# Kernel optimization log

Measured on AMD Instinct MI355X. Metric: run time of the kernel, lower is better.

## Reference

```python
import jax, jax.numpy as jnp
import numpy as np

NUM_HEADS = 32
HEAD_DIM = 128
ROPE_THETA = 10000.0


def setup_inputs() -> dict:
    key = jax.random.key(0)
    k1, k2, k3 = jax.random.split(key, 3)
    B, S, H = 2, 2048, 4096
    scale = 0.02
    return {
        "x": jax.random.normal(k1, (B, S, H), dtype=jnp.float32),
        "Wqkv": jax.random.normal(k2, (H, 3 * H), dtype=jnp.float32) * scale,
        "Wo": jax.random.normal(k3, (H, H), dtype=jnp.float32) * scale,
    }


def _rope_cos_sin(seq_len, head_dim, dtype):
    # inv_freq over even dims, llama convention
    inv_freq = 1.0 / (ROPE_THETA ** (jnp.arange(0, head_dim, 2, dtype=jnp.float32) / head_dim))
    t = jnp.arange(seq_len, dtype=jnp.float32)
    freqs = jnp.outer(t, inv_freq)            # [S, hd/2]
    emb = jnp.concatenate([freqs, freqs], -1)  # [S, hd]
    return jnp.cos(emb).astype(dtype), jnp.sin(emb).astype(dtype)


def _rotate_half(v):
    v1, v2 = jnp.split(v, 2, axis=-1)
    return jnp.concatenate([-v2, v1], axis=-1)


def _apply_rope(q, k, cos, sin):
    # q,k: [B,S,nh,hd]; cos,sin: [S,hd] -> broadcast over B and heads
    cos = cos[None, :, None, :]
    sin = sin[None, :, None, :]
    q = q * cos + _rotate_half(q) * sin
    k = k * cos + _rotate_half(k) * sin
    return q, k


def reference(x, Wqkv, Wo):
    B, S, H = x.shape
    nh, hd = NUM_HEADS, HEAD_DIM
    scaling = 1.0 / jnp.sqrt(jnp.asarray(hd, dtype=x.dtype))

    qkv = jnp.einsum("bsh,hk->bsk", x, Wqkv)           # fused QKV proj
    q, k, v = jnp.split(qkv, 3, axis=-1)
    q = q.reshape(B, S, nh, hd)
    k = k.reshape(B, S, nh, hd)
    v = v.reshape(B, S, nh, hd)

    cos, sin = _rope_cos_sin(S, hd, x.dtype)
    q, k = _apply_rope(q, k, cos, sin)

    # causal scaled dot-product attention
    scores = jnp.einsum("bqnd,bknd->bnqk", q, k) * scaling  # [B,nh,S,S]
    causal = jnp.tril(jnp.ones((S, S), dtype=bool))
    scores = jnp.where(causal[None, None], scores, jnp.finfo(scores.dtype).min)
    probs = jax.nn.softmax(scores, axis=-1)
    ctx = jnp.einsum("bnqk,bknd->bqnd", probs, v).reshape(B, S, nh * hd)

    return jnp.einsum("bsh,ho->bso", ctx, Wo)
```

## Files before the change

kernel.cpp:

```cpp
#include <hip/hip_runtime.h>

typedef __bf16 v8bf __attribute__((ext_vector_type(8)));
typedef float  v4f  __attribute__((ext_vector_type(4)));

__device__ __forceinline__ float bf2f(unsigned short h) {
    union { unsigned int u; float f; } x; x.u = ((unsigned int)h) << 16; return x.f;
}
__device__ __forceinline__ unsigned short f2bf(float f) {
    union { float f; unsigned int u; } x; x.f = f;
    unsigned int u = x.u;
    u += 0x7fffu + ((u >> 16) & 1u);
    return (unsigned short)(u >> 16);
}
__device__ __forceinline__ void gll16(const void* g, void* l) {
    __builtin_amdgcn_global_load_lds((__attribute__((address_space(1))) void*)g,
                                     (__attribute__((address_space(3))) void*)l,
                                     16, 0, 0);
}

__global__ __launch_bounds__(256) void cvt_f32_bf16(
    const float* __restrict__ in, unsigned short* __restrict__ out)
{
    size_t i = ((size_t)blockIdx.x * 256 + threadIdx.x) * 4;
    float4 v = *(const float4*)&in[i];
    ushort4 o;
    o.x = f2bf(v.x); o.y = f2bf(v.y); o.z = f2bf(v.z); o.w = f2bf(v.w);
    *(ushort4*)&out[i] = o;
}

__global__ __launch_bounds__(256) void transpose_f32_bf16(
    const float* __restrict__ in, unsigned short* __restrict__ out, int ldIn, int M)
{
    __shared__ unsigned short t[64][68];
    const int c0 = blockIdx.x * 64, r0 = blockIdx.y * 64;
    const int lr = threadIdx.x >> 4;
    const int lc = (threadIdx.x & 15) * 4;
#pragma unroll
    for (int i = 0; i < 4; ++i) {
        int row = lr + i * 16;
        float4 v = *(const float4*)&in[(size_t)(r0 + row) * ldIn + c0 + lc];
        ushort4 o;
        o.x = f2bf(v.x); o.y = f2bf(v.y); o.z = f2bf(v.z); o.w = f2bf(v.w);
        *(ushort4*)&t[row][lc] = o;
    }
    __syncthreads();
#pragma unroll
    for (int i = 0; i < 4; ++i) {
        int orow = lr + i * 16;
        ushort4 v;
        v.x = t[lc + 0][orow]; v.y = t[lc + 1][orow];
        v.z = t[lc + 2][orow]; v.w = t[lc + 3][orow];
        *(ushort4*)&out[(size_t)(c0 + orow) * M + r0 + lc] = v;
    }
}

template <int MODE>
__global__ __launch_bounds__(512, 2) void gemm256(
    const unsigned short* __restrict__ A, const unsigned short* __restrict__ Bt,
    float* __restrict__ Cf, unsigned short* __restrict__ Ov, float postScale)
{
    constexpr int NT = 64;
    __shared__ unsigned short lA[4 * 8192];
    __shared__ unsigned short lB[4 * 8192];
    const int tid = threadIdx.x;
    const int wave = tid >> 6, lane = tid & 63;
    const int quad = lane >> 4, l16 = lane & 15;
    const int wr = wave >> 2, wc = wave & 3;

    const int bid = blockIdx.x;
    const int swz = (bid & 7) * 32 + (bid >> 3);
    const int m0 = (swz >> 4) * 256, n0 = (swz & 15) * 256;

    v4f acc[8][4] = {};

    const int srow = tid >> 3;
    const int sof  = ((tid & 7) ^ (srow & 7)) << 3;
    const unsigned short* pA[2][2]; const unsigned short* pB[2][2];
#pragma unroll
    for (int H = 0; H < 2; ++H)
#pragma unroll
        for (int i = 0; i < 2; ++i) {
            pA[H][i] = A  + (size_t)(m0 + H * 128 + i * 64 + srow) * 4096 + sof;
            pB[H][i] = Bt + (size_t)(n0 + H * 128 + i * 64 + srow) * 4096 + sof;
        }
    const int dst0 = tid * 8;

    auto stA = [&](int H, int kt) {
        unsigned short* d = &lA[((kt & 1) * 2 + H) * 8192 + dst0];
        gll16(pA[H][0] + kt * 64, d);
        gll16(pA[H][1] + kt * 64, d + 4096);
    };
    auto stB = [&](int H, int kt) {
        unsigned short* d = &lB[((kt & 1) * 2 + H) * 8192 + dst0];
        gll16(pB[H][0] + kt * 64, d);
        gll16(pB[H][1] + kt * 64, d + 4096);
    };

    stB(0, 0); stB(1, 0); stA(0, 0); stA(1, 0);
    stB(0, 1); stB(1, 1); stA(0, 1);
    asm volatile("s_waitcnt vmcnt(6)" ::: "memory");
    __builtin_amdgcn_s_barrier();

    const int cko0 = (quad ^ (l16 & 7)) << 3;
    const int cko1 = ((4 + quad) ^ (l16 & 7)) << 3;
    const int arow0 = l16 * 64;
    const int brow0 = (wc * 16 + l16) * 64;

#pragma unroll 2
    for (int t = 0; t < NT; ++t) {
        const int c = t & 1;
        const unsigned short* lAc = &lA[(c * 2 + wr) * 8192];
        const unsigned short* lB0 = &lB[(c * 2 + 0) * 8192];
        const unsigned short* lB1 = &lB[(c * 2 + 1) * 8192];
        v8bf a[4][2], b0[2][2], b1[2][2];

#pragma unroll
        for (int mi = 0; mi < 4; ++mi) {
            a[mi][0] = *(const v8bf*)&lAc[arow0 + mi * 1024 + cko0];
            a[mi][1] = *(const v8bf*)&lAc[arow0 + mi * 1024 + cko1];
        }
#pragma unroll
        for (int ni = 0; ni < 2; ++ni) {
            b0[ni][0] = *(const v8bf*)&lB0[brow0 + ni * 4096 + cko0];
            b0[ni][1] = *(const v8bf*)&lB0[brow0 + ni * 4096 + cko1];
        }
        if (t + 1 < NT) stA(1, t + 1);
        __builtin_amdgcn_s_barrier();
        __builtin_amdgcn_s_setprio(1);
#pragma unroll
        for (int kc = 0; kc < 2; ++kc)
#pragma unroll
            for (int mi = 0; mi < 4; ++mi)
#pragma unroll
                for (int ni = 0; ni < 2; ++ni)
                    acc[mi][ni] = __builtin_amdgcn_mfma_f32_16x16x32_bf16(
                        a[mi][kc], b0[ni][kc], acc[mi][ni], 0, 0, 0);
        __builtin_amdgcn_s_setprio(0);
        __builtin_amdgcn_s_barrier();

#pragma unroll
        for (int ni = 0; ni < 2; ++ni) {
            b1[ni][0] = *(const v8bf*)&lB1[brow0 + ni * 4096 + cko0];
            b1[ni][1] = *(const v8bf*)&lB1[brow0 + ni * 4096 + cko1];
        }
        if (t + 2 < NT) stB(0, t + 2);
        __builtin_amdgcn_s_barrier();
        __builtin_amdgcn_s_setprio(1);
#pragma unroll
        for (int kc = 0; kc < 2; ++kc)
#pragma unroll
            for (int mi = 0; mi < 4; ++mi)
#pragma unroll
                for (int ni = 0; ni < 2; ++ni)
                    acc[mi][2 + ni] = __builtin_amdgcn_mfma_f32_16x16x32_bf16(
                        a[mi][kc], b1[ni][kc], acc[mi][2 + ni], 0, 0, 0);
        __builtin_amdgcn_s_setprio(0);
        __builtin_amdgcn_s_barrier();

#pragma unroll
        for (int mi = 0; mi < 4; ++mi) {
            a[mi][0] = *(const v8bf*)&lAc[arow0 + (4 + mi) * 1024 + cko0];
            a[mi][1] = *(const v8bf*)&lAc[arow0 + (4 + mi) * 1024 + cko1];
        }
        if (t + 2 < NT) stB(1, t + 2);
        __builtin_amdgcn_s_barrier();
        __builtin_amdgcn_s_setprio(1);
#pragma unroll
        for (int kc = 0; kc < 2; ++kc)
#pragma unroll
            for (int mi = 0; mi < 4; ++mi)
#pragma unroll
                for (int ni = 0; ni < 2; ++ni)
                    acc[4 + mi][2 + ni] = __builtin_amdgcn_mfma_f32_16x16x32_bf16(
                        a[mi][kc], b1[ni][kc], acc[4 + mi][2 + ni], 0, 0, 0);
        __builtin_amdgcn_s_setprio(0);
        __builtin_amdgcn_s_barrier();

        if (t + 2 < NT) {
            stA(0, t + 2);
            asm volatile("s_waitcnt vmcnt(6)" ::: "memory");
        } else if (t + 1 < NT) {
            asm volatile("s_waitcnt vmcnt(0)" ::: "memory");
        }
        __builtin_amdgcn_s_barrier();
        __builtin_amdgcn_s_setprio(1);
#pragma unroll
        for (int kc = 0; kc < 2; ++kc)
#pragma unroll
            for (int mi = 0; mi < 4; ++mi)
#pragma unroll
                for (int ni = 0; ni < 2; ++ni)
                    acc[4 + mi][ni] = __builtin_amdgcn_mfma_f32_16x16x32_bf16(
                        a[mi][kc], b0[ni][kc], acc[4 + mi][ni], 0, 0, 0);
        __builtin_amdgcn_s_setprio(0);
        __builtin_amdgcn_s_barrier();
    }

    if (MODE == 0) {
#pragma unroll
        for (int mi = 0; mi < 8; ++mi) {
            int gm = m0 + wr * 128 + mi * 16 + quad * 4;
#pragma unroll
            for (int ni = 0; ni < 4; ++ni) {
                int gn = n0 + ni * 64 + wc * 16 + l16;
#pragma unroll
                for (int r = 0; r < 4; ++r)
                    Cf[(size_t)(gm + r) * 4096 + gn] = acc[mi][ni][r];
            }
        }
    } else if (MODE == 1) {
        const int d1 = wc * 16 + l16;
        const float inv = powf(10000.0f, -(float)d1 * 0.015625f);
        const int head0 = n0 >> 7;
#pragma unroll
        for (int mi = 0; mi < 8; ++mi) {
            int gmb = m0 + wr * 128 + mi * 16 + quad * 4;
            int b = gmb >> 11, sb = gmb & 2047;
            float sn[4], cs[4];
#pragma unroll
            for (int r = 0; r < 4; ++r)
                sincosf((float)(sb + r) * inv, &sn[r], &cs[r]);
#pragma unroll
            for (int hd = 0; hd < 2; ++hd) {
                size_t hb = ((size_t)(b * 32 + head0 + hd)) << 11;
#pragma unroll
                for (int r = 0; r < 4; ++r) {
                    float x1 = acc[mi][2 * hd][r], x2 = acc[mi][2 * hd + 1][r];
                    size_t adr = (hb + sb + r) << 7;
                    Ov[adr + d1]      = f2bf((x1 * cs[r] - x2 * sn[r]) * postScale);
                    Ov[adr + d1 + 64] = f2bf((x2 * cs[r] + x1 * sn[r]) * postScale);
                }
            }
        }
    } else {
        const int head0 = n0 >> 7;
#pragma unroll
        for (int mi = 0; mi < 8; ++mi) {
            int gmb = m0 + wr * 128 + mi * 16 + quad * 4;
            int b = gmb >> 11, s0 = gmb & 2047;
#pragma unroll
            for (int ni = 0; ni < 4; ++ni) {
                int head = head0 + (ni >> 1);
                int d = ((ni & 1) << 6) + wc * 16 + l16;
                ushort4 o;
                o.x = f2bf(acc[mi][ni][0]); o.y = f2bf(acc[mi][ni][1]);
                o.z = f2bf(acc[mi][ni][2]); o.w = f2bf(acc[mi][ni][3]);
                *(ushort4*)&Ov[(((size_t)(b * 32 + head)) << 18) +
                               ((size_t)d << 11) + s0] = o;
            }
        }
    }
}

__global__ __launch_bounds__(256, 5) void attn_kernel(
    const unsigned short* __restrict__ Q, const unsigned short* __restrict__ Kg,
    const unsigned short* __restrict__ Vt, unsigned short* __restrict__ ctx)
{
    __shared__ unsigned short lK[2][32 * 128];
    __shared__ unsigned short lV[2][128 * 32];

    const int qt  = gridDim.x - 1 - blockIdx.x;
    const int bh  = blockIdx.y;
    const int tid = threadIdx.x;
    const int wave = tid >> 6, lane = tid & 63;
    const int quad = lane >> 4, l16 = lane & 15;
    const int q0 = qt * 64;
    const size_t base = (size_t)bh << 18;

    auto stage = [&](int kv0, int buf) {
#pragma unroll
        for (int it = 0; it < 2; ++it) {
            int cid = it * 256 + tid;
            int row = cid >> 4, chk = cid & 15;
            gll16(Kg + base + ((size_t)(kv0 + row) << 7) + ((chk ^ (row & 15)) << 3),
                  &lK[buf][cid << 3]);
        }
#pragma unroll
        for (int it = 0; it < 2; ++it) {
            int cid = it * 256 + tid;
            int row = cid >> 2, chk = cid & 3;
            gll16(Vt + base + ((size_t)row << 11) + kv0 + ((chk ^ ((row >> 1) & 3)) << 3),
                  &lV[buf][cid << 3]);
        }
    };

    v8bf qf[4];
    {
        const unsigned short* qrow =
            Q + base + ((size_t)(q0 + wave * 16 + l16) << 7) + quad * 8;
#pragma unroll
        for (int kc = 0; kc < 4; ++kc)
            qf[kc] = *(const v8bf*)(qrow + kc * 32);
    }

    const int qg = q0 + wave * 16 + l16;
    float mrow = -1e30f, lrow = 0.f;
    v4f Oa[8] = {};
    const float c2 = 1.4426950408889634f;
    const float thr = 4.1589045f;

    const int nkt = 2 * qt + 2;
    stage(0, 0);
    for (int kt = 0; kt < nkt; ++kt) {
        const int cur = kt & 1;
        __syncthreads();
        if (kt + 1 < nkt) stage((kt + 1) * 32, cur ^ 1);

        const unsigned short* K_ = &lK[cur][0];
        const unsigned short* V_ = &lV[cur][0];
        const int kv0 = kt * 32;

        v4f sc[2] = {};
        __builtin_amdgcn_s_setprio(1);
#pragma unroll
        for (int kc = 0; kc < 4; ++kc) {
#pragma unroll
            for (int nt = 0; nt < 2; ++nt) {
                v8bf kf = *(const v8bf*)&K_[((nt * 16 + l16) << 7) +
                                            ((((kc << 2) + quad) ^ l16) << 3)];
                sc[nt] = __builtin_amdgcn_mfma_f32_16x16x32_bf16(kf, qf[kc], sc[nt], 0, 0, 0);
            }
        }
        __builtin_amdgcn_s_setprio(0);

        if (kt >= nkt - 2) {
#pragma unroll
            for (int nt = 0; nt < 2; ++nt) {
                int kvb = kv0 + nt * 16 + quad * 4;
#pragma unroll
                for (int r = 0; r < 4; ++r)
                    if (kvb + r > qg) sc[nt][r] = -1e30f;
            }
        }

        float tmax = fmaxf(fmaxf(fmaxf(sc[0][0], sc[0][1]), fmaxf(sc[0][2], sc[0][3])),
                           fmaxf(fmaxf(sc[1][0], sc[1][1]), fmaxf(sc[1][2], sc[1][3])));
        tmax = fmaxf(tmax, __shfl_xor(tmax, 16));
        tmax = fmaxf(tmax, __shfl_xor(tmax, 32));

        if (__ballot(tmax > mrow + thr) != 0ull) {
            float mnew = fmaxf(mrow, tmax);
            float alpha = exp2f((mrow - mnew) * c2);
            mrow = mnew;
            lrow *= alpha;
#pragma unroll
            for (int d8 = 0; d8 < 8; ++d8)
#pragma unroll
                for (int r = 0; r < 4; ++r)
                    Oa[d8][r] *= alpha;
        }
        const float mc = mrow * c2;
        float rsum = 0.f;
#pragma unroll
        for (int nt = 0; nt < 2; ++nt)
#pragma unroll
            for (int r = 0; r < 4; ++r) {
                float p = exp2f(fmaf(sc[nt][r], c2, -mc));
                sc[nt][r] = p;
                rsum += p;
            }
        rsum += __shfl_xor(rsum, 16);
        rsum += __shfl_xor(rsum, 32);
        lrow += rsum;

        unsigned int pk0[2], pk1[2];
#pragma unroll
        for (int h = 0; h < 2; ++h) {
            pk0[h] = (unsigned int)f2bf(sc[0][2 * h]) |
                     ((unsigned int)f2bf(sc[0][2 * h + 1]) << 16);
            pk1[h] = (unsigned int)f2bf(sc[1][2 * h]) |
                     ((unsigned int)f2bf(sc[1][2 * h + 1]) << 16);
        }
        union { unsigned int u[4]; v8bf v; } pu;
        const int sbase = ((quad & 1) << 5) + l16;
#pragma unroll
        for (int j2 = 0; j2 < 4; ++j2) {
            int src = sbase + ((j2 >> 1) << 4);
            int a = __shfl((int)pk0[j2 & 1], src);
            int b = __shfl((int)pk1[j2 & 1], src);
            pu.u[j2] = (quad < 2) ? (unsigned int)a : (unsigned int)b;
        }
        v8bf pf = pu.v;

        __builtin_amdgcn_s_setprio(1);
#pragma unroll
        for (int dt = 0; dt < 8; ++dt) {
            v8bf vf = *(const v8bf*)&V_[((dt * 16 + l16) << 5) +
                                        ((quad ^ ((l16 >> 1) & 3)) << 3)];
            Oa[dt] = __builtin_amdgcn_mfma_f32_16x16x32_bf16(vf, pf, Oa[dt], 0, 0, 0);
        }
        __builtin_amdgcn_s_setprio(0);
    }

    const int b = bh >> 5, h = bh & 31;
    const float invl = 1.0f / lrow;
    size_t rowb = ((size_t)(b * 2048 + qg) << 12) + ((size_t)h << 7);
#pragma unroll
    for (int dt = 0; dt < 8; ++dt) {
        ushort4 o;
        o.x = f2bf(Oa[dt][0] * invl);
        o.y = f2bf(Oa[dt][1] * invl);
        o.z = f2bf(Oa[dt][2] * invl);
        o.w = f2bf(Oa[dt][3] * invl);
        *(ushort4*)&ctx[rowb + dt * 16 + quad * 4] = o;
    }
}

extern "C" void kernel_launch(void* const* d_in, const int* in_sizes, int n_in,
                              void* d_out, int out_size, void* d_ws, size_t ws_size,
                              hipStream_t stream)
{
    const float* x    = (const float*)d_in[0];
    const float* Wqkv = (const float*)d_in[1];
    const float* Wo   = (const float*)d_in[2];
    float* out = (float*)d_out;

    char* ws = (char*)d_ws;
    const size_t B32 = (size_t)32 * 1024 * 1024;
    unsigned short* B0 = (unsigned short*)(ws);
    unsigned short* B1 = (unsigned short*)(ws + 1 * B32);
    unsigned short* B2 = (unsigned short*)(ws + 2 * B32);
    unsigned short* B3 = (unsigned short*)(ws + 3 * B32);
    unsigned short* B4 = (unsigned short*)(ws + 4 * B32);

    const float qscale = 0.08838834764831845f;

    cvt_f32_bf16<<<16384, 256, 0, stream>>>(x, B0);
    transpose_f32_bf16<<<dim3(64, 64), 256, 0, stream>>>(Wqkv, B4, 12288, 4096);
    gemm256<1><<<256, 512, 0, stream>>>(B0, B4, nullptr, B1, qscale);
    transpose_f32_bf16<<<dim3(64, 64), 256, 0, stream>>>(Wqkv + 4096, B4, 12288, 4096);
    gemm256<1><<<256, 512, 0, stream>>>(B0, B4, nullptr, B2, 1.0f);
    transpose_f32_bf16<<<dim3(64, 64), 256, 0, stream>>>(Wqkv + 8192, B4, 12288, 4096);
    gemm256<2><<<256, 512, 0, stream>>>(B0, B4, nullptr, B3, 1.0f);
    transpose_f32_bf16<<<dim3(64, 64), 256, 0, stream>>>(Wo, B4, 4096, 4096);
    attn_kernel<<<dim3(32, 64), 256, 0, stream>>>(B1, B2, B3, B0);
    gemm256<0><<<256, 512, 0, stream>>>(B0, B4, out, nullptr, 1.0f);
}
```

Baseline: 1.066 ms.

## Fuse QKV GEMMs and weight transposes; process two Q tiles per attention block

The three Q/K/V projection GEMMs are merged into one 768-block launch whose epilogue routes each tile to Q, K or V by head group. The four weight transposes become a single launch, which cuts kernel launch count and lets the GEMM fill the GPU better. The attention kernel now handles 128 query rows per block as two 64-row groups that share each staged K/V tile, halving K/V loads per query. This raises register pressure (launch bounds drop to 3 blocks per CU), and the fused path needs 256 MB of workspace with a fallback to the old sequence.

```diff
diff --git a/kernel.cpp b/kernel.cpp
--- a/kernel.cpp
+++ b/kernel.cpp
@@ -51,6 +51,37 @@
         v.x = t[lc + 0][orow]; v.y = t[lc + 1][orow];
         v.z = t[lc + 2][orow]; v.w = t[lc + 3][orow];
         *(ushort4*)&out[(size_t)(c0 + orow) * M + r0 + lc] = v;
+    }
+}
+
+__global__ __launch_bounds__(256) void transpose_all(
+    const float* __restrict__ Wqkv, const float* __restrict__ Wo,
+    unsigned short* __restrict__ WT, unsigned short* __restrict__ WoT)
+{
+    __shared__ unsigned short t[64][68];
+    const int z = blockIdx.z;
+    const float* in = (z < 3) ? (Wqkv + z * 4096) : Wo;
+    unsigned short* out = (z < 3) ? (WT + (size_t)z * 16777216) : WoT;
+    const int ldIn = (z < 3) ? 12288 : 4096;
+    const int c0 = blockIdx.x * 64, r0 = blockIdx.y * 64;
+    const int lr = threadIdx.x >> 4;
+    const int lc = (threadIdx.x & 15) * 4;
+#pragma unroll
+    for (int i = 0; i < 4; ++i) {
+        int row = lr + i * 16;
+        float4 v = *(const float4*)&in[(size_t)(r0 + row) * ldIn + c0 + lc];
+        ushort4 o;
+        o.x = f2bf(v.x); o.y = f2bf(v.y); o.z = f2bf(v.z); o.w = f2bf(v.w);
+        *(ushort4*)&t[row][lc] = o;
+    }
+    __syncthreads();
+#pragma unroll
+    for (int i = 0; i < 4; ++i) {
+        int orow = lr + i * 16;
+        ushort4 v;
+        v.x = t[lc + 0][orow]; v.y = t[lc + 1][orow];
+        v.z = t[lc + 2][orow]; v.w = t[lc + 3][orow];
+        *(ushort4*)&out[(size_t)(c0 + orow) * 4096 + r0 + lc] = v;
     }
 }
 
@@ -68,8 +99,14 @@
     const int wr = wave >> 2, wc = wave & 3;
 
     const int bid = blockIdx.x;
-    const int swz = (bid & 7) * 32 + (bid >> 3);
-    const int m0 = (swz >> 4) * 256, n0 = (swz & 15) * 256;
+    int m0, n0;
+    if (MODE == 3) {
+        const int swz = (bid & 7) * 96 + (bid >> 3);
+        m0 = (swz / 48) * 256; n0 = (swz % 48) * 256;
+    } else {
+        const int swz = (bid & 7) * 32 + (bid >> 3);
+        m0 = (swz >> 4) * 256; n0 = (swz & 15) * 256;
+    }
 
     v4f acc[8][4] = {};
 
@@ -208,51 +245,57 @@
                     Cf[(size_t)(gm + r) * 4096 + gn] = acc[mi][ni][r];
             }
         }
-    } else if (MODE == 1) {
-        const int d1 = wc * 16 + l16;
-        const float inv = powf(10000.0f, -(float)d1 * 0.015625f);
-        const int head0 = n0 >> 7;
-#pragma unroll
-        for (int mi = 0; mi < 8; ++mi) {
-            int gmb = m0 + wr * 128 + mi * 16 + quad * 4;
-            int b = gmb >> 11, sb = gmb & 2047;
-            float sn[4], cs[4];
-#pragma unroll
-            for (int r = 0; r < 4; ++r)
-                sincosf((float)(sb + r) * inv, &sn[r], &cs[r]);
-#pragma unroll
-            for (int hd = 0; hd < 2; ++hd) {
-                size_t hb = ((size_t)(b * 32 + head0 + hd)) << 11;
-#pragma unroll
-                for (int r = 0; r < 4; ++r) {
-                    float x1 = acc[mi][2 * hd][r], x2 = acc[mi][2 * hd + 1][r];
-                    size_t adr = (hb + sb + r) << 7;
-                    Ov[adr + d1]      = f2bf((x1 * cs[r] - x2 * sn[r]) * postScale);
-                    Ov[adr + d1 + 64] = f2bf((x2 * cs[r] + x1 * sn[r]) * postScale);
-                }
-            }
-        }
     } else {
-        const int head0 = n0 >> 7;
-#pragma unroll
-        for (int mi = 0; mi < 8; ++mi) {
-            int gmb = m0 + wr * 128 + mi * 16 + quad * 4;
-            int b = gmb >> 11, s0 = gmb & 2047;
-#pragma unroll
-            for (int ni = 0; ni < 4; ++ni) {
-                int head = head0 + (ni >> 1);
-                int d = ((ni & 1) << 6) + wc * 16 + l16;
-                ushort4 o;
-                o.x = f2bf(acc[mi][ni][0]); o.y = f2bf(acc[mi][ni][1]);
-                o.z = f2bf(acc[mi][ni][2]); o.w = f2bf(acc[mi][ni][3]);
-                *(ushort4*)&Ov[(((size_t)(b * 32 + head)) << 18) +
-                               ((size_t)d << 11) + s0] = o;
-            }
-        }
-    }
-}
-
-__global__ __launch_bounds__(256, 5) void attn_kernel(
+        const int head0g = n0 >> 7;
+        const int hg = (MODE == 3) ? (head0g >> 5) : (MODE == 2 ? 2 : 0);
+        const int headl = head0g & 31;
+        if (hg == 2) {
+            unsigned short* Vo = (MODE == 3) ? Ov + 33554432 : Ov;
+#pragma unroll
+            for (int mi = 0; mi < 8; ++mi) {
+                int gmb = m0 + wr * 128 + mi * 16 + quad * 4;
+                int b = gmb >> 11, s0 = gmb & 2047;
+#pragma unroll
+                for (int ni = 0; ni < 4; ++ni) {
+                    int head = headl + (ni >> 1);
+                    int d = ((ni & 1) << 6) + wc * 16 + l16;
+                    ushort4 o;
+                    o.x = f2bf(acc[mi][ni][0]); o.y = f2bf(acc[mi][ni][1]);
+                    o.z = f2bf(acc[mi][ni][2]); o.w = f2bf(acc[mi][ni][3]);
+                    *(ushort4*)&Vo[(((size_t)(b * 32 + head)) << 18) +
+                                   ((size_t)d << 11) + s0] = o;
+                }
+            }
+        } else {
+            unsigned short* Qo = (MODE == 3 && hg == 1) ? Ov + 16777216 : Ov;
+            const float scl = (MODE == 3 && hg == 1) ? 1.0f : postScale;
+            const int d1 = wc * 16 + l16;
+            const float inv = powf(10000.0f, -(float)d1 * 0.015625f);
+#pragma unroll
+            for (int mi = 0; mi < 8; ++mi) {
+                int gmb = m0 + wr * 128 + mi * 16 + quad * 4;
+                int b = gmb >> 11, sb = gmb & 2047;
+                float sn[4], cs[4];
+#pragma unroll
+                for (int r = 0; r < 4; ++r)
+                    sincosf((float)(sb + r) * inv, &sn[r], &cs[r]);
+#pragma unroll
+                for (int hd = 0; hd < 2; ++hd) {
+                    size_t hb = ((size_t)(b * 32 + headl + hd)) << 11;
+#pragma unroll
+                    for (int r = 0; r < 4; ++r) {
+                        float x1 = acc[mi][2 * hd][r], x2 = acc[mi][2 * hd + 1][r];
+                        size_t adr = (hb + sb + r) << 7;
+                        Qo[adr + d1]      = f2bf((x1 * cs[r] - x2 * sn[r]) * scl);
+                        Qo[adr + d1 + 64] = f2bf((x2 * cs[r] + x1 * sn[r]) * scl);
+                    }
+                }
+            }
+        }
+    }
+}
+
+__global__ __launch_bounds__(256, 3) void attn_kernel(
     const unsigned short* __restrict__ Q, const unsigned short* __restrict__ Kg,
     const unsigned short* __restrict__ Vt, unsigned short* __restrict__ ctx)
 {
@@ -264,7 +307,7 @@
     const int tid = threadIdx.x;
     const int wave = tid >> 6, lane = tid & 63;
     const int quad = lane >> 4, l16 = lane & 15;
-    const int q0 = qt * 64;
+    const int q0 = qt * 128;
     const size_t base = (size_t)bh << 18;
 
     auto stage = [&](int kv0, int buf) {
@@ -284,22 +327,26 @@
         }
     };
 
-    v8bf qf[4];
+    v8bf qf0[4], qf1[4];
     {
         const unsigned short* qrow =
             Q + base + ((size_t)(q0 + wave * 16 + l16) << 7) + quad * 8;
 #pragma unroll
-        for (int kc = 0; kc < 4; ++kc)
-            qf[kc] = *(const v8bf*)(qrow + kc * 32);
-    }
-
-    const int qg = q0 + wave * 16 + l16;
-    float mrow = -1e30f, lrow = 0.f;
-    v4f Oa[8] = {};
+        for (int kc = 0; kc < 4; ++kc) {
+            qf0[kc] = *(const v8bf*)(qrow + kc * 32);
+            qf1[kc] = *(const v8bf*)(qrow + 8192 + kc * 32);
+        }
+    }
+
+    const int qg0 = q0 + wave * 16 + l16;
+    const int qg1 = qg0 + 64;
+    float m0r = -1e30f, l0r = 0.f, m1r = -1e30f, l1r = 0.f;
+    v4f Oa0[8] = {}, Oa1[8] = {};
     const float c2 = 1.4426950408889634f;
     const float thr = 4.1589045f;
-
-    const int nkt = 2 * qt + 2;
+    const int sbase = ((quad & 1) << 5) + l16;
+
+    const int nkt = 4 * qt + 4;
     stage(0, 0);
     for (int kt = 0; kt < nkt; ++kt) {
         const int cur = kt & 1;
@@ -309,100 +356,178 @@
         const unsigned short* K_ = &lK[cur][0];
         const unsigned short* V_ = &lV[cur][0];
         const int kv0 = kt * 32;
-
-        v4f sc[2] = {};
+        const bool g0live = (kt < nkt - 2);
+
+        v4f sc0[2] = {}, sc1[2] = {};
         __builtin_amdgcn_s_setprio(1);
-#pragma unroll
-        for (int kc = 0; kc < 4; ++kc) {
-#pragma unroll
-            for (int nt = 0; nt < 2; ++nt) {
-                v8bf kf = *(const v8bf*)&K_[((nt * 16 + l16) << 7) +
-                                            ((((kc << 2) + quad) ^ l16) << 3)];
-                sc[nt] = __builtin_amdgcn_mfma_f32_16x16x32_bf16(kf, qf[kc], sc[nt], 0, 0, 0);
-            }
+        if (g0live) {
+#pragma unroll
+            for (int kc = 0; kc < 4; ++kc)
+#pragma unroll
+                for (int nt = 0; nt < 2; ++nt) {
+                    v8bf kf = *(const v8bf*)&K_[((nt * 16 + l16) << 7) +
+                                                ((((kc << 2) + quad) ^ l16) << 3)];
+                    sc0[nt] = __builtin_amdgcn_mfma_f32_16x16x32_bf16(kf, qf0[kc], sc0[nt], 0, 0, 0);
+                    sc1[nt] = __builtin_amdgcn_mfma_f32_16x16x32_bf16(kf, qf1[kc], sc1[nt], 0, 0, 0);
+                }
+        } else {
+#pragma unroll
+            for (int kc = 0; kc < 4; ++kc)
+#pragma unroll
+                for (int nt = 0; nt < 2; ++nt) {
+                    v8bf kf = *(const v8bf*)&K_[((nt * 16 + l16) << 7) +
+                                                ((((kc << 2) + quad) ^ l16) << 3)];
+                    sc1[nt] = __builtin_amdgcn_mfma_f32_16x16x32_bf16(kf, qf1[kc], sc1[nt], 0, 0, 0);
+                }
         }
         __builtin_amdgcn_s_setprio(0);
 
-        if (kt >= nkt - 2) {
-#pragma unroll
-            for (int nt = 0; nt < 2; ++nt) {
-                int kvb = kv0 + nt * 16 + quad * 4;
-#pragma unroll
-                for (int r = 0; r < 4; ++r)
-                    if (kvb + r > qg) sc[nt][r] = -1e30f;
-            }
-        }
-
-        float tmax = fmaxf(fmaxf(fmaxf(sc[0][0], sc[0][1]), fmaxf(sc[0][2], sc[0][3])),
-                           fmaxf(fmaxf(sc[1][0], sc[1][1]), fmaxf(sc[1][2], sc[1][3])));
-        tmax = fmaxf(tmax, __shfl_xor(tmax, 16));
-        tmax = fmaxf(tmax, __shfl_xor(tmax, 32));
-
-        if (__ballot(tmax > mrow + thr) != 0ull) {
-            float mnew = fmaxf(mrow, tmax);
-            float alpha = exp2f((mrow - mnew) * c2);
-            mrow = mnew;
-            lrow *= alpha;
-#pragma unroll
-            for (int d8 = 0; d8 < 8; ++d8)
-#pragma unroll
-                for (int r = 0; r < 4; ++r)
-                    Oa[d8][r] *= alpha;
-        }
-        const float mc = mrow * c2;
-        float rsum = 0.f;
-#pragma unroll
-        for (int nt = 0; nt < 2; ++nt)
-#pragma unroll
-            for (int r = 0; r < 4; ++r) {
-                float p = exp2f(fmaf(sc[nt][r], c2, -mc));
-                sc[nt][r] = p;
-                rsum += p;
-            }
-        rsum += __shfl_xor(rsum, 16);
-        rsum += __shfl_xor(rsum, 32);
-        lrow += rsum;
-
-        unsigned int pk0[2], pk1[2];
-#pragma unroll
-        for (int h = 0; h < 2; ++h) {
-            pk0[h] = (unsigned int)f2bf(sc[0][2 * h]) |
-                     ((unsigned int)f2bf(sc[0][2 * h + 1]) << 16);
-            pk1[h] = (unsigned int)f2bf(sc[1][2 * h]) |
-                     ((unsigned int)f2bf(sc[1][2 * h + 1]) << 16);
-        }
-        union { unsigned int u[4]; v8bf v; } pu;
-        const int sbase = ((quad & 1) << 5) + l16;
-#pragma unroll
-        for (int j2 = 0; j2 < 4; ++j2) {
-            int src = sbase + ((j2 >> 1) << 4);
-            int a = __shfl((int)pk0[j2 & 1], src);
-            int b = __shfl((int)pk1[j2 & 1], src);
-            pu.u[j2] = (quad < 2) ? (unsigned int)a : (unsigned int)b;
-        }
-        v8bf pf = pu.v;
+        union { unsigned int u[4]; v8bf v; } pu0, pu1;
+
+        if (g0live) {
+            if (kt >= nkt - 4) {
+#pragma unroll
+                for (int nt = 0; nt < 2; ++nt) {
+                    int kvb = kv0 + nt * 16 + quad * 4;
+#pragma unroll
+                    for (int r = 0; r < 4; ++r)
+                        if (kvb + r > qg0) sc0[nt][r] = -1e30f;
+                }
+            }
+            float tmax = fmaxf(fmaxf(fmaxf(sc0[0][0], sc0[0][1]), fmaxf(sc0[0][2], sc0[0][3])),
+                               fmaxf(fmaxf(sc0[1][0], sc0[1][1]), fmaxf(sc0[1][2], sc0[1][3])));
+            tmax = fmaxf(tmax, __shfl_xor(tmax, 16));
+            tmax = fmaxf(tmax, __shfl_xor(tmax, 32));
+            if (__ballot(tmax > m0r + thr) != 0ull) {
+                float mnew = fmaxf(m0r, tmax);
+                float alpha = exp2f((m0r - mnew) * c2);
+                m0r = mnew;
+                l0r *= alpha;
+#pragma unroll
+                for (int d8 = 0; d8 < 8; ++d8)
+#pragma unroll
+                    for (int r = 0; r < 4; ++r)
+                        Oa0[d8][r] *= alpha;
+            }
+            const float mc = m0r * c2;
+            float rsum = 0.f;
+#pragma unroll
+            for (int nt = 0; nt < 2; ++nt)
+#pragma unroll
+                for (int r = 0; r < 4; ++r) {
+                    float p = exp2f(fmaf(sc0[nt][r], c2, -mc));
+                    sc0[nt][r] = p;
+                    rsum += p;
+                }
+            rsum += __shfl_xor(rsum, 16);
+            rsum += __shfl_xor(rsum, 32);
+            l0r += rsum;
+
+            unsigned int pk0[2], pk1[2];
+#pragma unroll
+            for (int h = 0; h < 2; ++h) {
+                pk0[h] = (unsigned int)f2bf(sc0[0][2 * h]) |
+                         ((unsigned int)f2bf(sc0[0][2 * h + 1]) << 16);
+                pk1[h] = (unsigned int)f2bf(sc0[1][2 * h]) |
+                         ((unsigned int)f2bf(sc0[1][2 * h + 1]) << 16);
+            }
+#pragma unroll
+            for (int j2 = 0; j2 < 4; ++j2) {
+                int src = sbase + ((j2 >> 1) << 4);
+                int a = __shfl((int)pk0[j2 & 1], src);
+                int b = __shfl((int)pk1[j2 & 1], src);
+                pu0.u[j2] = (quad < 2) ? (unsigned int)a : (unsigned int)b;
+            }
+        } else {
+            pu0.u[0] = 0; pu0.u[1] = 0; pu0.u[2] = 0; pu0.u[3] = 0;
+        }
+
+        {
+            if (kt >= nkt - 2) {
+#pragma unroll
+                for (int nt = 0; nt < 2; ++nt) {
+                    int kvb = kv0 + nt * 16 + quad * 4;
+#pragma unroll
+                    for (int r = 0; r < 4; ++r)
+                        if (kvb + r > qg1) sc1[nt][r] = -1e30f;
+                }
+            }
+            float tmax = fmaxf(fmaxf(fmaxf(sc1[0][0], sc1[0][1]), fmaxf(sc1[0][2], sc1[0][3])),
+                               fmaxf(fmaxf(sc1[1][0], sc1[1][1]), fmaxf(sc1[1][2], sc1[1][3])));
+            tmax = fmaxf(tmax, __shfl_xor(tmax, 16));
+            tmax = fmaxf(tmax, __shfl_xor(tmax, 32));
+            if (__ballot(tmax > m1r + thr) != 0ull) {
+                float mnew = fmaxf(m1r, tmax);
+                float alpha = exp2f((m1r - mnew) * c2);
+                m1r = mnew;
+                l1r *= alpha;
+#pragma unroll
+                for (int d8 = 0; d8 < 8; ++d8)
+#pragma unroll
+                    for (int r = 0; r < 4; ++r)
+                        Oa1[d8][r] *= alpha;
+            }
+            const float mc = m1r * c2;
+            float rsum = 0.f;
+#pragma unroll
+            for (int nt = 0; nt < 2; ++nt)
+#pragma unroll
+                for (int r = 0; r < 4; ++r) {
+                    float p = exp2f(fmaf(sc1[nt][r], c2, -mc));
+                    sc1[nt][r] = p;
+                    rsum += p;
+                }
+            rsum += __shfl_xor(rsum, 16);
+            rsum += __shfl_xor(rsum, 32);
+            l1r += rsum;
+
+            unsigned int pk0[2], pk1[2];
+#pragma unroll
+            for (int h = 0; h < 2; ++h) {
+                pk0[h] = (unsigned int)f2bf(sc1[0][2 * h]) |
+                         ((unsigned int)f2bf(sc1[0][2 * h + 1]) << 16);
+                pk1[h] = (unsigned int)f2bf(sc1[1][2 * h]) |
+                         ((unsigned int)f2bf(sc1[1][2 * h + 1]) << 16);
+            }
+#pragma unroll
+            for (int j2 = 0; j2 < 4; ++j2) {
+                int src = sbase + ((j2 >> 1) << 4);
+                int a = __shfl((int)pk0[j2 & 1], src);
+                int b = __shfl((int)pk1[j2 & 1], src);
+                pu1.u[j2] = (quad < 2) ? (unsigned int)a : (unsigned int)b;
+            }
+        }
+        v8bf pf0 = pu0.v, pf1 = pu1.v;
 
         __builtin_amdgcn_s_setprio(1);
 #pragma unroll
         for (int dt = 0; dt < 8; ++dt) {
             v8bf vf = *(const v8bf*)&V_[((dt * 16 + l16) << 5) +
                                         ((quad ^ ((l16 >> 1) & 3)) << 3)];
-            Oa[dt] = __builtin_amdgcn_mfma_f32_16x16x32_bf16(vf, pf, Oa[dt], 0, 0, 0);
+            Oa0[dt] = __builtin_amdgcn_mfma_f32_16x16x32_bf16(vf, pf0, Oa0[dt], 0, 0, 0);
+            Oa1[dt] = __builtin_amdgcn_mfma_f32_16x16x32_bf16(vf, pf1, Oa1[dt], 0, 0, 0);
         }
         __builtin_amdgcn_s_setprio(0);
     }
 
     const int b = bh >> 5, h = bh & 31;
-    const float invl = 1.0f / lrow;
-    size_t rowb = ((size_t)(b * 2048 + qg) << 12) + ((size_t)h << 7);
+    const float invl0 = 1.0f / l0r, invl1 = 1.0f / l1r;
+    size_t rowb0 = ((size_t)(b * 2048 + qg0) << 12) + ((size_t)h << 7);
+    size_t rowb1 = rowb0 + ((size_t)64 << 12);
 #pragma unroll
     for (int dt = 0; dt < 8; ++dt) {
         ushort4 o;
-        o.x = f2bf(Oa[dt][0] * invl);
-        o.y = f2bf(Oa[dt][1] * invl);
-        o.z = f2bf(Oa[dt][2] * invl);
-        o.w = f2bf(Oa[dt][3] * invl);
-        *(ushort4*)&ctx[rowb + dt * 16 + quad * 4] = o;
+        o.x = f2bf(Oa0[dt][0] * invl0);
+        o.y = f2bf(Oa0[dt][1] * invl0);
+        o.z = f2bf(Oa0[dt][2] * invl0);
+        o.w = f2bf(Oa0[dt][3] * invl0);
+        *(ushort4*)&ctx[rowb0 + dt * 16 + quad * 4] = o;
+        ushort4 p;
+        p.x = f2bf(Oa1[dt][0] * invl1);
+        p.y = f2bf(Oa1[dt][1] * invl1);
+        p.z = f2bf(Oa1[dt][2] * invl1);
+        p.w = f2bf(Oa1[dt][3] * invl1);
+        *(ushort4*)&ctx[rowb1 + dt * 16 + quad * 4] = p;
     }
 }
 
@@ -421,18 +546,28 @@
     unsigned short* B1 = (unsigned short*)(ws + 1 * B32);
     unsigned short* B2 = (unsigned short*)(ws + 2 * B32);
     unsigned short* B3 = (unsigned short*)(ws + 3 * B32);
-    unsigned short* B4 = (unsigned short*)(ws + 4 * B32);
 
     const float qscale = 0.08838834764831845f;
 
-    cvt_f32_bf16<<<16384, 256, 0, stream>>>(x, B0);
-    transpose_f32_bf16<<<dim3(64, 64), 256, 0, stream>>>(Wqkv, B4, 12288, 4096);
-    gemm256<1><<<256, 512, 0, stream>>>(B0, B4, nullptr, B1, qscale);
-    transpose_f32_bf16<<<dim3(64, 64), 256, 0, stream>>>(Wqkv + 4096, B4, 12288, 4096);
-    gemm256<1><<<256, 512, 0, stream>>>(B0, B4, nullptr, B2, 1.0f);
-    transpose_f32_bf16<<<dim3(64, 64), 256, 0, stream>>>(Wqkv + 8192, B4, 12288, 4096);
-    gemm256<2><<<256, 512, 0, stream>>>(B0, B4, nullptr, B3, 1.0f);
-    transpose_f32_bf16<<<dim3(64, 64), 256, 0, stream>>>(Wo, B4, 4096, 4096);
-    attn_kernel<<<dim3(32, 64), 256, 0, stream>>>(B1, B2, B3, B0);
-    gemm256<0><<<256, 512, 0, stream>>>(B0, B4, out, nullptr, 1.0f);
-}
+    if (ws_size >= (size_t)256 * 1024 * 1024) {
+        unsigned short* WT  = (unsigned short*)(ws + 4 * B32);
+        unsigned short* WoT = (unsigned short*)(ws + 7 * B32);
+        cvt_f32_bf16<<<16384, 256, 0, stream>>>(x, B0);
+        transpose_all<<<dim3(64, 64, 4), 256, 0, stream>>>(Wqkv, Wo, WT, WoT);
+        gemm256<3><<<768, 512, 0, stream>>>(B0, WT, nullptr, B1, qscale);
+        attn_kernel<<<dim3(16, 64), 256, 0, stream>>>(B1, B2, B3, B0);
+        gemm256<0><<<256, 512, 0, stream>>>(B0, WoT, out, nullptr, 1.0f);
+    } else {
+        unsigned short* B4 = (unsigned short*)(ws + 4 * B32);
+        cvt_f32_bf16<<<16384, 256, 0, stream>>>(x, B0);
+        transpose_f32_bf16<<<dim3(64, 64), 256, 0, stream>>>(Wqkv, B4, 12288, 4096);
+        gemm256<1><<<256, 512, 0, stream>>>(B0, B4, nullptr, B1, qscale);
+        transpose_f32_bf16<<<dim3(64, 64), 256, 0, stream>>>(Wqkv + 4096, B4, 12288, 4096);
+        gemm256<1><<<256, 512, 0, stream>>>(B0, B4, nullptr, B2, 1.0f);
+        transpose_f32_bf16<<<dim3(64, 64), 256, 0, stream>>>(Wqkv + 8192, B4, 12288, 4096);
+        gemm256<2><<<256, 512, 0, stream>>>(B0, B4, nullptr, B3, 1.0f);
+        transpose_f32_bf16<<<dim3(64, 64), 256, 0, stream>>>(Wo, B4, 4096, 4096);
+        attn_kernel<<<dim3(16, 64), 256, 0, stream>>>(B1, B2, B3, B0);
+        gemm256<0><<<256, 512, 0, stream>>>(B0, B4, out, nullptr, 1.0f);
+    }
+}
```

Measured after the change: 1.113 ms. +4.4%, slower.
